# Kernel tuning notes

Measured on AMD Instinct MI355X. Metric: run time of the kernel, lower is better.

## Reference

```python
import jax, jax.numpy as jnp
import numpy as np

FEAT = 320        # in_channel == out_channel, LayerNorm dim
NPTS = 2048       # num_points == Conv1d channels (proj_dim)
TEMP = FEAT ** 0.5
EPS = 1e-5


def setup_inputs() -> dict:
    key = jax.random.key(0)
    ks = jax.random.split(key, 7)
    B = 32
    query = jax.random.normal(ks[0], (B, FEAT, NPTS), dtype=jnp.float32)
    support = jax.random.normal(ks[1], (B, FEAT, NPTS), dtype=jnp.float32)
    # Conv1d(2048, 2048, 1, bias=False) weights, squeezed to [out, in]
    s = 1.0 / np.sqrt(NPTS)
    Wq = jax.random.uniform(ks[2], (NPTS, NPTS), jnp.float32, -s, s)
    Wk = jax.random.uniform(ks[3], (NPTS, NPTS), jnp.float32, -s, s)
    Wv = jax.random.uniform(ks[4], (NPTS, NPTS), jnp.float32, -s, s)
    gamma = jnp.ones((FEAT,), jnp.float32)
    beta = jnp.zeros((FEAT,), jnp.float32)
    return {"query": query, "support": support, "Wq": Wq, "Wk": Wk,
            "Wv": Wv, "gamma": gamma, "beta": beta}


def reference(query, support, Wq, Wk, Wv, gamma, beta):
    # query, support: [B, FEAT=320, NPTS=2048]
    # 1x1 Conv1d on x.transpose(1,2) -> q[b,o,l] = sum_i W[o,i] * x[b,l,i]
    q = jnp.einsum('oi,bfi->bof', Wq, support)   # [B, NPTS, FEAT]
    k = jnp.einsum('oi,bfi->bof', Wk, query)     # [B, NPTS, FEAT]
    v = jnp.einsum('oi,bfi->bof', Wv, query)     # [B, NPTS, FEAT]
    # attn[b,l,m] = sum_o q[b,o,l] * k[b,o,m] / sqrt(FEAT)
    attn = jnp.einsum('bol,bom->blm', q, k) / TEMP   # [B, FEAT, FEAT]
    attn = jax.nn.softmax(attn, axis=-1)
    # query_output[b,l,o] = sum_m attn[b,l,m] * v[b,o,m]
    query_output = jnp.einsum('blm,bom->blo', attn, v)  # [B, FEAT, NPTS]
    # residual + LayerNorm over the FEAT (=320) axis
    up = (query_output + query).transpose(0, 2, 1)      # [B, NPTS, FEAT]
    mu = jnp.mean(up, axis=-1, keepdims=True)
    var = jnp.var(up, axis=-1, keepdims=True)
    normed = (up - mu) * jax.lax.rsqrt(var + EPS) * gamma + beta
    return normed.transpose(0, 2, 1)                    # [B, FEAT, NPTS]
```

## Files before the change

kernel.cpp:

```cpp
#include <hip/hip_runtime.h>

typedef _Float16 f16;
typedef _Float16 f16x4 __attribute__((ext_vector_type(4)));
typedef _Float16 f16x8 __attribute__((ext_vector_type(8)));
typedef float    f32x4 __attribute__((ext_vector_type(4)));

#define NB    32
#define FEAT  320
#define NPTS  2048
#define M1    (NB * FEAT)
#define KDIM  2048

__device__ __forceinline__ void stage16(f16* lds_base, const f16* g, int lane) {
#if defined(__has_builtin) && __has_builtin(__builtin_amdgcn_global_load_lds)
    __builtin_amdgcn_global_load_lds(
        (const __attribute__((address_space(1))) void*)g,
        (__attribute__((address_space(3))) void*)lds_base, 16, 0, 0);
#else
    *(f16x8*)(lds_base + lane * 8) = *(const f16x8*)g;
#endif
}

__global__ void cast_k(const float* __restrict__ src, f16* __restrict__ dst, int n4) {
    int i = blockIdx.x * blockDim.x + threadIdx.x;
    int stride = gridDim.x * blockDim.x;
    for (; i < n4; i += stride) {
        f32x4 v = *(const f32x4*)(src + (size_t)i * 4);
        f16x4 h = __builtin_convertvector(v, f16x4);
        *(f16x4*)(dst + (size_t)i * 4) = h;
    }
}

__global__ __launch_bounds__(256, 2) void gemm1_k(
    const f16* __restrict__ sq, const f16* __restrict__ qr,
    const f16* __restrict__ wq, const f16* __restrict__ wk, const f16* __restrict__ wv,
    f16* __restrict__ qq, f16* __restrict__ kk, f16* __restrict__ vv) {
    __shared__ f16 As[128 * 32];
    __shared__ f16 Bs[128 * 32];
    const int z = blockIdx.z;
    const f16* A = (z == 0) ? sq : qr;
    const f16* W = (z == 0) ? wq : (z == 1) ? wk : wv;
    f16* C       = (z == 0) ? qq : (z == 1) ? kk : vv;

    const int tid  = threadIdx.x;
    const int lane = tid & 63;
    const int w    = tid >> 6;
    const int wm   = w >> 1, wn = w & 1;
    const int lo   = lane & 15, q4 = lane >> 4;
    const long tm = (long)blockIdx.y * 128;
    const long tn = (long)blockIdx.x * 128;
    const f16* Abase = A + tm * KDIM;
    const f16* Bbase = W + tn * KDIM;

    f32x4 acc[4][4] = {};
    const int e0 = w * 64 + lane;

    for (int k0 = 0; k0 < KDIM; k0 += 32) {
#pragma unroll
        for (int j = 0; j < 2; ++j) {
            int e = j * 256 + e0;
            int row = e >> 2, ch = e & 3;
            stage16(&As[j * 2048 + w * 512], Abase + (long)row * KDIM + k0 + ch * 8, lane);
            stage16(&Bs[j * 2048 + w * 512], Bbase + (long)row * KDIM + k0 + ch * 8, lane);
        }
        __syncthreads();
        f16x8 af[4], bf[4];
#pragma unroll
        for (int mi = 0; mi < 4; ++mi)
            af[mi] = *(const f16x8*)&As[(wm * 64 + mi * 16 + lo) * 32 + q4 * 8];
#pragma unroll
        for (int ni = 0; ni < 4; ++ni)
            bf[ni] = *(const f16x8*)&Bs[(wn * 64 + ni * 16 + lo) * 32 + q4 * 8];
#pragma unroll
        for (int mi = 0; mi < 4; ++mi)
#pragma unroll
            for (int ni = 0; ni < 4; ++ni)
                acc[mi][ni] = __builtin_amdgcn_mfma_f32_16x16x32_f16(af[mi], bf[ni], acc[mi][ni], 0, 0, 0);
        __syncthreads();
    }
#pragma unroll
    for (int mi = 0; mi < 4; ++mi)
#pragma unroll
        for (int ni = 0; ni < 4; ++ni) {
            long gc = tn + wn * 64 + ni * 16 + lo;
#pragma unroll
            for (int r = 0; r < 4; ++r) {
                long gr = tm + wm * 64 + mi * 16 + q4 * 4 + r;
                C[gr * KDIM + gc] = (f16)acc[mi][ni][r];
            }
        }
}

__global__ void transpose_v(const f16* __restrict__ vv, f16* __restrict__ vT) {
    __shared__ f16 T[64][80];
    const int b = blockIdx.z;
    const int f0 = blockIdx.y * 64, o0 = blockIdx.x * 64;
    const int tid = threadIdx.x;
#pragma unroll
    for (int j = 0; j < 2; ++j) {
        int e = tid * 2 + j;
        int r = e >> 3, c = e & 7;
        *(f16x8*)&T[r][c * 8] =
            *(const f16x8*)&vv[((size_t)b * FEAT + f0 + r) * NPTS + o0 + c * 8];
    }
    __syncthreads();
#pragma unroll
    for (int j = 0; j < 2; ++j) {
        int e = tid * 2 + j;
        int o = e >> 3, fc = e & 7;
        f16x8 val;
#pragma unroll
        for (int jj = 0; jj < 8; ++jj) val[jj] = T[fc * 8 + jj][o];
        *(f16x8*)&vT[(size_t)b * (NPTS * FEAT) + (size_t)(o0 + o) * FEAT + f0 + fc * 8] = val;
    }
}

__global__ __launch_bounds__(256, 2) void attn_gemm(
    const f16* __restrict__ qq, const f16* __restrict__ kk, float* __restrict__ attn) {
    __shared__ f16 As[64 * 32];
    __shared__ f16 Bs[64 * 32];
    const int b = blockIdx.z;
    const long tl = (long)blockIdx.y * 64, tmm = (long)blockIdx.x * 64;
    const int tid = threadIdx.x, lane = tid & 63, w = tid >> 6;
    const int wm = w >> 1, wn = w & 1, lo = lane & 15, q4 = lane >> 4;
    const f16* Abase = qq + ((long)b * FEAT + tl) * KDIM;
    const f16* Bbase = kk + ((long)b * FEAT + tmm) * KDIM;
    const int e = w * 64 + lane, row = e >> 2, ch = e & 3;

    f32x4 acc[2][2] = {};
    for (int k0 = 0; k0 < KDIM; k0 += 32) {
        stage16(&As[w * 512], Abase + (long)row * KDIM + k0 + ch * 8, lane);
        stage16(&Bs[w * 512], Bbase + (long)row * KDIM + k0 + ch * 8, lane);
        __syncthreads();
        f16x8 af[2], bf[2];
#pragma unroll
        for (int mi = 0; mi < 2; ++mi)
            af[mi] = *(const f16x8*)&As[(wm * 32 + mi * 16 + lo) * 32 + q4 * 8];
#pragma unroll
        for (int ni = 0; ni < 2; ++ni)
            bf[ni] = *(const f16x8*)&Bs[(wn * 32 + ni * 16 + lo) * 32 + q4 * 8];
#pragma unroll
        for (int mi = 0; mi < 2; ++mi)
#pragma unroll
            for (int ni = 0; ni < 2; ++ni)
                acc[mi][ni] = __builtin_amdgcn_mfma_f32_16x16x32_f16(af[mi], bf[ni], acc[mi][ni], 0, 0, 0);
        __syncthreads();
    }
    const float scale = 0.05590169943749474f;
#pragma unroll
    for (int mi = 0; mi < 2; ++mi)
#pragma unroll
        for (int ni = 0; ni < 2; ++ni) {
            long gm = tmm + wn * 32 + ni * 16 + lo;
#pragma unroll
            for (int r = 0; r < 4; ++r) {
                long gl = tl + wm * 32 + mi * 16 + q4 * 4 + r;
                attn[(long)b * (FEAT * FEAT) + gl * FEAT + gm] = acc[mi][ni][r] * scale;
            }
        }
}

__global__ void softmax_k(const float* __restrict__ attn, f16* __restrict__ probs) {
    const int r = blockIdx.x * 4 + (threadIdx.x >> 6);
    const int lane = threadIdx.x & 63;
    const float* row = attn + (size_t)r * FEAT;
    float v[5];
    float mx = -1e30f;
#pragma unroll
    for (int j = 0; j < 5; ++j) { v[j] = row[lane + j * 64]; mx = fmaxf(mx, v[j]); }
#pragma unroll
    for (int off = 32; off; off >>= 1) mx = fmaxf(mx, __shfl_xor(mx, off, 64));
    float s = 0.f;
#pragma unroll
    for (int j = 0; j < 5; ++j) { v[j] = __expf(v[j] - mx); s += v[j]; }
#pragma unroll
    for (int off = 32; off; off >>= 1) s += __shfl_xor(s, off, 64);
    const float inv = 1.f / s;
    f16* prow = probs + (size_t)r * FEAT;
#pragma unroll
    for (int j = 0; j < 5; ++j) prow[lane + j * 64] = (f16)(v[j] * inv);
}

__global__ __launch_bounds__(256, 2) void pv_gemm(
    const f16* __restrict__ probs, const f16* __restrict__ vT,
    const float* __restrict__ query, float* __restrict__ out) {
    __shared__ f16 As[64 * 32];
    __shared__ f16 Bs[64 * 32];
    const int b = blockIdx.z;
    const long tl = (long)blockIdx.y * 64, to = (long)blockIdx.x * 64;
    const int tid = threadIdx.x, lane = tid & 63, w = tid >> 6;
    const int wm = w >> 1, wn = w & 1, lo = lane & 15, q4 = lane >> 4;
    const f16* Abase = probs + (long)b * (FEAT * FEAT) + tl * FEAT;
    const f16* Bbase = vT + (long)b * (NPTS * FEAT) + to * FEAT;
    const int e = w * 64 + lane, row = e >> 2, ch = e & 3;

    f32x4 acc[2][2] = {};
    for (int k0 = 0; k0 < FEAT; k0 += 32) {
        stage16(&As[w * 512], Abase + (long)row * FEAT + k0 + ch * 8, lane);
        stage16(&Bs[w * 512], Bbase + (long)row * FEAT + k0 + ch * 8, lane);
        __syncthreads();
        f16x8 af[2], bf[2];
#pragma unroll
        for (int mi = 0; mi < 2; ++mi)
            af[mi] = *(const f16x8*)&As[(wm * 32 + mi * 16 + lo) * 32 + q4 * 8];
#pragma unroll
        for (int ni = 0; ni < 2; ++ni)
            bf[ni] = *(const f16x8*)&Bs[(wn * 32 + ni * 16 + lo) * 32 + q4 * 8];
#pragma unroll
        for (int mi = 0; mi < 2; ++mi)
#pragma unroll
            for (int ni = 0; ni < 2; ++ni)
                acc[mi][ni] = __builtin_amdgcn_mfma_f32_16x16x32_f16(af[mi], bf[ni], acc[mi][ni], 0, 0, 0);
        __syncthreads();
    }
#pragma unroll
    for (int mi = 0; mi < 2; ++mi)
#pragma unroll
        for (int ni = 0; ni < 2; ++ni) {
            long go = to + wn * 32 + ni * 16 + lo;
#pragma unroll
            for (int r = 0; r < 4; ++r) {
                long gl = tl + wm * 32 + mi * 16 + q4 * 4 + r;
                size_t idx = (size_t)b * (FEAT * NPTS) + (size_t)gl * NPTS + go;
                out[idx] = acc[mi][ni][r] + query[idx];
            }
        }
}

__global__ void ln_k(float* __restrict__ out, const float* __restrict__ gamma,
                     const float* __restrict__ beta) {
    __shared__ float g[FEAT], bt[FEAT];
    const int tid = threadIdx.x;
    for (int i = tid; i < FEAT; i += 256) { g[i] = gamma[i]; bt[i] = beta[i]; }
    __syncthreads();
    const int col = blockIdx.x * 256 + tid;
    const int b = col >> 11, o = col & 2047;
    float* base = out + (size_t)b * (FEAT * NPTS) + o;
    float s = 0.f, ss = 0.f;
    for (int l = 0; l < FEAT; ++l) {
        float x = base[(size_t)l * NPTS];
        s += x; ss += x * x;
    }
    const float mu = s * (1.f / FEAT);
    const float var = ss * (1.f / FEAT) - mu * mu;
    const float rstd = rsqrtf(var + 1e-5f);
    for (int l = 0; l < FEAT; ++l) {
        float x = base[(size_t)l * NPTS];
        base[(size_t)l * NPTS] = (x - mu) * rstd * g[l] + bt[l];
    }
}

extern "C" void kernel_launch(void* const* d_in, const int* in_sizes, int n_in,
                              void* d_out, int out_size, void* d_ws, size_t ws_size,
                              hipStream_t stream) {
    const float* query   = (const float*)d_in[0];
    const float* support = (const float*)d_in[1];
    const float* Wq      = (const float*)d_in[2];
    const float* Wk      = (const float*)d_in[3];
    const float* Wv      = (const float*)d_in[4];
    const float* gamma   = (const float*)d_in[5];
    const float* beta    = (const float*)d_in[6];
    float* out = (float*)d_out;

    char* ws = (char*)d_ws;
    const size_t SZ_X = (size_t)M1 * KDIM * sizeof(f16);
    const size_t SZ_W = (size_t)KDIM * KDIM * sizeof(f16);
    f16* sq = (f16*)(ws);
    f16* qr = (f16*)(ws + SZ_X);
    f16* wq = (f16*)(ws + 2 * SZ_X);
    f16* wk = (f16*)(ws + 2 * SZ_X + SZ_W);
    f16* wv = (f16*)(ws + 2 * SZ_X + 2 * SZ_W);
    f16* qq = (f16*)(ws + 2 * SZ_X + 3 * SZ_W);
    f16* kk = (f16*)(ws + 3 * SZ_X + 3 * SZ_W);
    f16* vv = (f16*)(ws + 4 * SZ_X + 3 * SZ_W);
    f16*   vT    = sq;
    float* attn  = (float*)(ws + SZ_X);
    f16*   probs = (f16*)(ws + SZ_X + (size_t)NB * FEAT * FEAT * 4);

    const int nX4 = (M1 * KDIM) / 4;
    const int nW4 = (KDIM * KDIM) / 4;
    cast_k<<<2048, 256, 0, stream>>>(support, sq, nX4);
    cast_k<<<2048, 256, 0, stream>>>(query, qr, nX4);
    cast_k<<<1024, 256, 0, stream>>>(Wq, wq, nW4);
    cast_k<<<1024, 256, 0, stream>>>(Wk, wk, nW4);
    cast_k<<<1024, 256, 0, stream>>>(Wv, wv, nW4);

    gemm1_k<<<dim3(16, 80, 3), 256, 0, stream>>>(sq, qr, wq, wk, wv, qq, kk, vv);
    transpose_v<<<dim3(32, 5, 32), 256, 0, stream>>>(vv, vT);
    attn_gemm<<<dim3(5, 5, 32), 256, 0, stream>>>(qq, kk, attn);
    softmax_k<<<2560, 256, 0, stream>>>(attn, probs);
    pv_gemm<<<dim3(32, 5, 32), 256, 0, stream>>>(probs, vT, query, out);
    ln_k<<<256, 256, 0, stream>>>(out, gamma, beta);
}
```

Baseline: 779.5 us.

## Reassociate attention to fold Wq/Wk into one matrix and apply Wv last

Reorders the projection matmuls. A combined matrix G = Wk^T·Wq (scaled by 1/temp) is built once, then T = support·G, so the attention logits come from T against the raw query, and the separate Q and K projections disappear. The Wv projection moves after P·query, so only two large batched 2048-wide GEMMs remain instead of three, and the V transpose kernel is removed. This adds a weight-weight GEMM, a dual-layout query cast, and longer fp16 product chains that could change rounding.

```diff
diff --git a/kernel.cpp b/kernel.cpp
--- a/kernel.cpp
+++ b/kernel.cpp
@@ -12,13 +12,9 @@
 #define KDIM  2048
 
 __device__ __forceinline__ void stage16(f16* lds_base, const f16* g, int lane) {
-#if defined(__has_builtin) && __has_builtin(__builtin_amdgcn_global_load_lds)
     __builtin_amdgcn_global_load_lds(
         (const __attribute__((address_space(1))) void*)g,
         (__attribute__((address_space(3))) void*)lds_base, 16, 0, 0);
-#else
-    *(f16x8*)(lds_base + lane * 8) = *(const f16x8*)g;
-#endif
 }
 
 __global__ void cast_k(const float* __restrict__ src, f16* __restrict__ dst, int n4) {
@@ -26,40 +22,75 @@
     int stride = gridDim.x * blockDim.x;
     for (; i < n4; i += stride) {
         f32x4 v = *(const f32x4*)(src + (size_t)i * 4);
-        f16x4 h = __builtin_convertvector(v, f16x4);
-        *(f16x4*)(dst + (size_t)i * 4) = h;
-    }
-}
-
-__global__ __launch_bounds__(256, 2) void gemm1_k(
-    const f16* __restrict__ sq, const f16* __restrict__ qr,
-    const f16* __restrict__ wq, const f16* __restrict__ wk, const f16* __restrict__ wv,
-    f16* __restrict__ qq, f16* __restrict__ kk, f16* __restrict__ vv) {
+        *(f16x4*)(dst + (size_t)i * 4) = __builtin_convertvector(v, f16x4);
+    }
+}
+
+__global__ void castT_k(const float* __restrict__ Wq, const float* __restrict__ Wk,
+                        f16* __restrict__ WqT, f16* __restrict__ WkT) {
+    __shared__ float T[64][65];
+    const float* W = blockIdx.z ? Wk : Wq;
+    f16* WT        = blockIdx.z ? WkT : WqT;
+    const int i0 = blockIdx.x * 64, o0 = blockIdx.y * 64;
+    const int tid = threadIdx.x;
+#pragma unroll
+    for (int j = 0; j < 4; ++j) {
+        int e = j * 256 + tid, r = e >> 4, c4 = e & 15;
+        f32x4 v = *(const f32x4*)&W[(size_t)(o0 + r) * 2048 + i0 + c4 * 4];
+        *(f32x4*)&T[r][c4 * 4] = v;
+    }
+    __syncthreads();
+#pragma unroll
+    for (int j = 0; j < 2; ++j) {
+        int e = j * 256 + tid, ir = e >> 3, oc8 = e & 7;
+        f16x8 val;
+#pragma unroll
+        for (int k = 0; k < 8; ++k) val[k] = (f16)T[oc8 * 8 + k][ir];
+        *(f16x8*)&WT[(size_t)(i0 + ir) * 2048 + o0 + oc8 * 8] = val;
+    }
+}
+
+__global__ void cast_q_dual(const float* __restrict__ q, f16* __restrict__ qf16,
+                            f16* __restrict__ qT16) {
+    __shared__ float T[64][65];
+    const int b = blockIdx.z;
+    const int j0 = blockIdx.x * 64, m0 = blockIdx.y * 64;
+    const int tid = threadIdx.x;
+#pragma unroll
+    for (int j = 0; j < 4; ++j) {
+        int e = j * 256 + tid, r = e >> 4, c4 = e & 15;
+        size_t src = ((size_t)b * FEAT + m0 + r) * NPTS + j0 + c4 * 4;
+        f32x4 v = *(const f32x4*)&q[src];
+        *(f32x4*)&T[r][c4 * 4] = v;
+        *(f16x4*)&qf16[src] = __builtin_convertvector(v, f16x4);
+    }
+    __syncthreads();
+#pragma unroll
+    for (int j = 0; j < 2; ++j) {
+        int e = j * 256 + tid, jr = e >> 3, mc8 = e & 7;
+        f16x8 val;
+#pragma unroll
+        for (int k = 0; k < 8; ++k) val[k] = (f16)T[mc8 * 8 + k][jr];
+        *(f16x8*)&qT16[((size_t)b * NPTS + j0 + jr) * FEAT + m0 + mc8 * 8] = val;
+    }
+}
+
+__global__ __launch_bounds__(256, 2) void gemm128_f16(
+    const f16* __restrict__ A, const f16* __restrict__ B, f16* __restrict__ C,
+    float scale) {
     __shared__ f16 As[128 * 32];
     __shared__ f16 Bs[128 * 32];
-    const int z = blockIdx.z;
-    const f16* A = (z == 0) ? sq : qr;
-    const f16* W = (z == 0) ? wq : (z == 1) ? wk : wv;
-    f16* C       = (z == 0) ? qq : (z == 1) ? kk : vv;
-
-    const int tid  = threadIdx.x;
-    const int lane = tid & 63;
-    const int w    = tid >> 6;
-    const int wm   = w >> 1, wn = w & 1;
-    const int lo   = lane & 15, q4 = lane >> 4;
-    const long tm = (long)blockIdx.y * 128;
-    const long tn = (long)blockIdx.x * 128;
+    const int tid = threadIdx.x, lane = tid & 63, w = tid >> 6;
+    const int wm = w >> 1, wn = w & 1, lo = lane & 15, q4 = lane >> 4;
+    const long tm = (long)blockIdx.y * 128, tn = (long)blockIdx.x * 128;
     const f16* Abase = A + tm * KDIM;
-    const f16* Bbase = W + tn * KDIM;
-
+    const f16* Bbase = B + tn * KDIM;
     f32x4 acc[4][4] = {};
     const int e0 = w * 64 + lane;
-
     for (int k0 = 0; k0 < KDIM; k0 += 32) {
 #pragma unroll
         for (int j = 0; j < 2; ++j) {
-            int e = j * 256 + e0;
-            int row = e >> 2, ch = e & 3;
+            int e = j * 256 + e0, row = e >> 2, ch = e & 3;
             stage16(&As[j * 2048 + w * 512], Abase + (long)row * KDIM + k0 + ch * 8, lane);
             stage16(&Bs[j * 2048 + w * 512], Bbase + (long)row * KDIM + k0 + ch * 8, lane);
         }
@@ -86,47 +117,70 @@
 #pragma unroll
             for (int r = 0; r < 4; ++r) {
                 long gr = tm + wm * 64 + mi * 16 + q4 * 4 + r;
-                C[gr * KDIM + gc] = (f16)acc[mi][ni][r];
+                C[gr * KDIM + gc] = (f16)(acc[mi][ni][r] * scale);
             }
         }
 }
 
-__global__ void transpose_v(const f16* __restrict__ vv, f16* __restrict__ vT) {
-    __shared__ f16 T[64][80];
-    const int b = blockIdx.z;
-    const int f0 = blockIdx.y * 64, o0 = blockIdx.x * 64;
-    const int tid = threadIdx.x;
-#pragma unroll
-    for (int j = 0; j < 2; ++j) {
-        int e = tid * 2 + j;
-        int r = e >> 3, c = e & 7;
-        *(f16x8*)&T[r][c * 8] =
-            *(const f16x8*)&vv[((size_t)b * FEAT + f0 + r) * NPTS + o0 + c * 8];
-    }
-    __syncthreads();
-#pragma unroll
-    for (int j = 0; j < 2; ++j) {
-        int e = tid * 2 + j;
-        int o = e >> 3, fc = e & 7;
-        f16x8 val;
-#pragma unroll
-        for (int jj = 0; jj < 8; ++jj) val[jj] = T[fc * 8 + jj][o];
-        *(f16x8*)&vT[(size_t)b * (NPTS * FEAT) + (size_t)(o0 + o) * FEAT + f0 + fc * 8] = val;
-    }
+__global__ __launch_bounds__(256, 2) void gemm128_res(
+    const f16* __restrict__ A, const f16* __restrict__ B,
+    const float* __restrict__ query, float* __restrict__ out) {
+    __shared__ f16 As[128 * 32];
+    __shared__ f16 Bs[128 * 32];
+    const int tid = threadIdx.x, lane = tid & 63, w = tid >> 6;
+    const int wm = w >> 1, wn = w & 1, lo = lane & 15, q4 = lane >> 4;
+    const long tm = (long)blockIdx.y * 128, tn = (long)blockIdx.x * 128;
+    const f16* Abase = A + tm * KDIM;
+    const f16* Bbase = B + tn * KDIM;
+    f32x4 acc[4][4] = {};
+    const int e0 = w * 64 + lane;
+    for (int k0 = 0; k0 < KDIM; k0 += 32) {
+#pragma unroll
+        for (int j = 0; j < 2; ++j) {
+            int e = j * 256 + e0, row = e >> 2, ch = e & 3;
+            stage16(&As[j * 2048 + w * 512], Abase + (long)row * KDIM + k0 + ch * 8, lane);
+            stage16(&Bs[j * 2048 + w * 512], Bbase + (long)row * KDIM + k0 + ch * 8, lane);
+        }
+        __syncthreads();
+        f16x8 af[4], bf[4];
+#pragma unroll
+        for (int mi = 0; mi < 4; ++mi)
+            af[mi] = *(const f16x8*)&As[(wm * 64 + mi * 16 + lo) * 32 + q4 * 8];
+#pragma unroll
+        for (int ni = 0; ni < 4; ++ni)
+            bf[ni] = *(const f16x8*)&Bs[(wn * 64 + ni * 16 + lo) * 32 + q4 * 8];
+#pragma unroll
+        for (int mi = 0; mi < 4; ++mi)
+#pragma unroll
+            for (int ni = 0; ni < 4; ++ni)
+                acc[mi][ni] = __builtin_amdgcn_mfma_f32_16x16x32_f16(af[mi], bf[ni], acc[mi][ni], 0, 0, 0);
+        __syncthreads();
+    }
+#pragma unroll
+    for (int mi = 0; mi < 4; ++mi)
+#pragma unroll
+        for (int ni = 0; ni < 4; ++ni) {
+            long gc = tn + wn * 64 + ni * 16 + lo;
+#pragma unroll
+            for (int r = 0; r < 4; ++r) {
+                long gr = tm + wm * 64 + mi * 16 + q4 * 4 + r;
+                size_t idx = (size_t)gr * KDIM + gc;
+                out[idx] = acc[mi][ni][r] + query[idx];
+            }
+        }
 }
 
 __global__ __launch_bounds__(256, 2) void attn_gemm(
-    const f16* __restrict__ qq, const f16* __restrict__ kk, float* __restrict__ attn) {
+    const f16* __restrict__ T, const f16* __restrict__ qf16, float* __restrict__ attn) {
     __shared__ f16 As[64 * 32];
     __shared__ f16 Bs[64 * 32];
     const int b = blockIdx.z;
     const long tl = (long)blockIdx.y * 64, tmm = (long)blockIdx.x * 64;
     const int tid = threadIdx.x, lane = tid & 63, w = tid >> 6;
     const int wm = w >> 1, wn = w & 1, lo = lane & 15, q4 = lane >> 4;
-    const f16* Abase = qq + ((long)b * FEAT + tl) * KDIM;
-    const f16* Bbase = kk + ((long)b * FEAT + tmm) * KDIM;
+    const f16* Abase = T + ((long)b * FEAT + tl) * KDIM;
+    const f16* Bbase = qf16 + ((long)b * FEAT + tmm) * KDIM;
     const int e = w * 64 + lane, row = e >> 2, ch = e & 3;
-
     f32x4 acc[2][2] = {};
     for (int k0 = 0; k0 < KDIM; k0 += 32) {
         stage16(&As[w * 512], Abase + (long)row * KDIM + k0 + ch * 8, lane);
@@ -146,7 +200,6 @@
                 acc[mi][ni] = __builtin_amdgcn_mfma_f32_16x16x32_f16(af[mi], bf[ni], acc[mi][ni], 0, 0, 0);
         __syncthreads();
     }
-    const float scale = 0.05590169943749474f;
 #pragma unroll
     for (int mi = 0; mi < 2; ++mi)
 #pragma unroll
@@ -155,7 +208,50 @@
 #pragma unroll
             for (int r = 0; r < 4; ++r) {
                 long gl = tl + wm * 32 + mi * 16 + q4 * 4 + r;
-                attn[(long)b * (FEAT * FEAT) + gl * FEAT + gm] = acc[mi][ni][r] * scale;
+                attn[(long)b * (FEAT * FEAT) + gl * FEAT + gm] = acc[mi][ni][r];
+            }
+        }
+}
+
+__global__ __launch_bounds__(256, 2) void u_gemm(
+    const f16* __restrict__ P, const f16* __restrict__ qT16, f16* __restrict__ U) {
+    __shared__ f16 As[64 * 32];
+    __shared__ f16 Bs[64 * 32];
+    const int b = blockIdx.z;
+    const long tl = (long)blockIdx.y * 64, to = (long)blockIdx.x * 64;
+    const int tid = threadIdx.x, lane = tid & 63, w = tid >> 6;
+    const int wm = w >> 1, wn = w & 1, lo = lane & 15, q4 = lane >> 4;
+    const f16* Abase = P + ((long)b * FEAT + tl) * FEAT;
+    const f16* Bbase = qT16 + ((long)b * NPTS + to) * FEAT;
+    const int e = w * 64 + lane, row = e >> 2, ch = e & 3;
+    f32x4 acc[2][2] = {};
+    for (int k0 = 0; k0 < FEAT; k0 += 32) {
+        stage16(&As[w * 512], Abase + (long)row * FEAT + k0 + ch * 8, lane);
+        stage16(&Bs[w * 512], Bbase + (long)row * FEAT + k0 + ch * 8, lane);
+        __syncthreads();
+        f16x8 af[2], bf[2];
+#pragma unroll
+        for (int mi = 0; mi < 2; ++mi)
+            af[mi] = *(const f16x8*)&As[(wm * 32 + mi * 16 + lo) * 32 + q4 * 8];
+#pragma unroll
+        for (int ni = 0; ni < 2; ++ni)
+            bf[ni] = *(const f16x8*)&Bs[(wn * 32 + ni * 16 + lo) * 32 + q4 * 8];
+#pragma unroll
+        for (int mi = 0; mi < 2; ++mi)
+#pragma unroll
+            for (int ni = 0; ni < 2; ++ni)
+                acc[mi][ni] = __builtin_amdgcn_mfma_f32_16x16x32_f16(af[mi], bf[ni], acc[mi][ni], 0, 0, 0);
+        __syncthreads();
+    }
+#pragma unroll
+    for (int mi = 0; mi < 2; ++mi)
+#pragma unroll
+        for (int ni = 0; ni < 2; ++ni) {
+            long go = to + wn * 32 + ni * 16 + lo;
+#pragma unroll
+            for (int r = 0; r < 4; ++r) {
+                long gl = tl + wm * 32 + mi * 16 + q4 * 4 + r;
+                U[((long)b * FEAT + gl) * NPTS + go] = (f16)acc[mi][ni][r];
             }
         }
 }
@@ -179,52 +275,6 @@
     f16* prow = probs + (size_t)r * FEAT;
 #pragma unroll
     for (int j = 0; j < 5; ++j) prow[lane + j * 64] = (f16)(v[j] * inv);
-}
-
-__global__ __launch_bounds__(256, 2) void pv_gemm(
-    const f16* __restrict__ probs, const f16* __restrict__ vT,
-    const float* __restrict__ query, float* __restrict__ out) {
-    __shared__ f16 As[64 * 32];
-    __shared__ f16 Bs[64 * 32];
-    const int b = blockIdx.z;
-    const long tl = (long)blockIdx.y * 64, to = (long)blockIdx.x * 64;
-    const int tid = threadIdx.x, lane = tid & 63, w = tid >> 6;
-    const int wm = w >> 1, wn = w & 1, lo = lane & 15, q4 = lane >> 4;
-    const f16* Abase = probs + (long)b * (FEAT * FEAT) + tl * FEAT;
-    const f16* Bbase = vT + (long)b * (NPTS * FEAT) + to * FEAT;
-    const int e = w * 64 + lane, row = e >> 2, ch = e & 3;
-
-    f32x4 acc[2][2] = {};
-    for (int k0 = 0; k0 < FEAT; k0 += 32) {
-        stage16(&As[w * 512], Abase + (long)row * FEAT + k0 + ch * 8, lane);
-        stage16(&Bs[w * 512], Bbase + (long)row * FEAT + k0 + ch * 8, lane);
-        __syncthreads();
-        f16x8 af[2], bf[2];
-#pragma unroll
-        for (int mi = 0; mi < 2; ++mi)
-            af[mi] = *(const f16x8*)&As[(wm * 32 + mi * 16 + lo) * 32 + q4 * 8];
-#pragma unroll
-        for (int ni = 0; ni < 2; ++ni)
-            bf[ni] = *(const f16x8*)&Bs[(wn * 32 + ni * 16 + lo) * 32 + q4 * 8];
-#pragma unroll
-        for (int mi = 0; mi < 2; ++mi)
-#pragma unroll
-            for (int ni = 0; ni < 2; ++ni)
-                acc[mi][ni] = __builtin_amdgcn_mfma_f32_16x16x32_f16(af[mi], bf[ni], acc[mi][ni], 0, 0, 0);
-        __syncthreads();
-    }
-#pragma unroll
-    for (int mi = 0; mi < 2; ++mi)
-#pragma unroll
-        for (int ni = 0; ni < 2; ++ni) {
-            long go = to + wn * 32 + ni * 16 + lo;
-#pragma unroll
-            for (int r = 0; r < 4; ++r) {
-                long gl = tl + wm * 32 + mi * 16 + q4 * 4 + r;
-                size_t idx = (size_t)b * (FEAT * NPTS) + (size_t)gl * NPTS + go;
-                out[idx] = acc[mi][ni][r] + query[idx];
-            }
-        }
 }
 
 __global__ void ln_k(float* __restrict__ out, const float* __restrict__ gamma,
@@ -263,32 +313,32 @@
     float* out = (float*)d_out;
 
     char* ws = (char*)d_ws;
+    const size_t SZ_W = (size_t)KDIM * KDIM * sizeof(f16);
     const size_t SZ_X = (size_t)M1 * KDIM * sizeof(f16);
-    const size_t SZ_W = (size_t)KDIM * KDIM * sizeof(f16);
-    f16* sq = (f16*)(ws);
-    f16* qr = (f16*)(ws + SZ_X);
-    f16* wq = (f16*)(ws + 2 * SZ_X);
-    f16* wk = (f16*)(ws + 2 * SZ_X + SZ_W);
-    f16* wv = (f16*)(ws + 2 * SZ_X + 2 * SZ_W);
-    f16* qq = (f16*)(ws + 2 * SZ_X + 3 * SZ_W);
-    f16* kk = (f16*)(ws + 3 * SZ_X + 3 * SZ_W);
-    f16* vv = (f16*)(ws + 4 * SZ_X + 3 * SZ_W);
-    f16*   vT    = sq;
-    float* attn  = (float*)(ws + SZ_X);
-    f16*   probs = (f16*)(ws + SZ_X + (size_t)NB * FEAT * FEAT * 4);
-
-    const int nX4 = (M1 * KDIM) / 4;
-    const int nW4 = (KDIM * KDIM) / 4;
-    cast_k<<<2048, 256, 0, stream>>>(support, sq, nX4);
-    cast_k<<<2048, 256, 0, stream>>>(query, qr, nX4);
-    cast_k<<<1024, 256, 0, stream>>>(Wq, wq, nW4);
-    cast_k<<<1024, 256, 0, stream>>>(Wk, wk, nW4);
-    cast_k<<<1024, 256, 0, stream>>>(Wv, wv, nW4);
-
-    gemm1_k<<<dim3(16, 80, 3), 256, 0, stream>>>(sq, qr, wq, wk, wv, qq, kk, vv);
-    transpose_v<<<dim3(32, 5, 32), 256, 0, stream>>>(vv, vT);
-    attn_gemm<<<dim3(5, 5, 32), 256, 0, stream>>>(qq, kk, attn);
-    softmax_k<<<2560, 256, 0, stream>>>(attn, probs);
-    pv_gemm<<<dim3(32, 5, 32), 256, 0, stream>>>(probs, vT, query, out);
+    f16* wqT  = (f16*)(ws);
+    f16* wkT  = (f16*)(ws + SZ_W);
+    f16* wv16 = (f16*)(ws + 2 * SZ_W);
+    f16* gt   = (f16*)(ws + 3 * SZ_W);
+    f16* sf16 = (f16*)(ws + 4 * SZ_W);
+    f16* qf16 = (f16*)(ws + 4 * SZ_W + SZ_X);
+    f16* qT16 = (f16*)(ws + 4 * SZ_W + 2 * SZ_X);
+    f16* T    = (f16*)(ws + 4 * SZ_W + 3 * SZ_X);
+    float* attn = (float*)(ws);
+    f16*   P    = qf16;
+    f16*   U    = sf16;
+
+    const float inv_temp = 0.05590169943749474f;
+
+    castT_k<<<dim3(32, 32, 2), 256, 0, stream>>>(Wq, Wk, wqT, wkT);
+    cast_k<<<1024, 256, 0, stream>>>(Wv, wv16, (KDIM * KDIM) / 4);
+    cast_k<<<2048, 256, 0, stream>>>(support, sf16, (M1 * KDIM) / 4);
+    cast_q_dual<<<dim3(32, 5, 32), 256, 0, stream>>>(query, qf16, qT16);
+
+    gemm128_f16<<<dim3(16, 16), 256, 0, stream>>>(wkT, wqT, gt, inv_temp);
+    gemm128_f16<<<dim3(16, 80), 256, 0, stream>>>(sf16, gt, T, 1.0f);
+    attn_gemm<<<dim3(5, 5, 32), 256, 0, stream>>>(T, qf16, attn);
+    softmax_k<<<2560, 256, 0, stream>>>(attn, P);
+    u_gemm<<<dim3(32, 5, 32), 256, 0, stream>>>(P, qT16, U);
+    gemm128_res<<<dim3(16, 80), 256, 0, stream>>>(U, wv16, query, out);
     ln_k<<<256, 256, 0, stream>>>(out, gamma, beta);
 }
```

Result: faster. 740.9 us (-4.9%).
